# Kernel tuning notes

Measured on AMD Instinct MI355X. Metric: run time of the kernel, lower is better.

The kernel has to match this reference:

```python
import jax, jax.numpy as jnp
import numpy as np

N, DIM, HEADS, DH, WS = 32768, 1024, 8, 64, 256
INNER = HEADS * DH
MASK_VAL = -1e10  # ATTN_MASK_VALUE
EPS = 1e-5


def setup_inputs() -> dict:
    key = jax.random.key(0)
    k0, k1, k2 = jax.random.split(key, 3)
    x = jax.random.normal(k0, (N, DIM), jnp.float32)
    # rotary sin/cos with interleaved-pair layout matching rotate_every_two
    inv_freq = 1.0 / (10000.0 ** (jnp.arange(0, DH, 2, dtype=jnp.float32) / DH))
    freqs = jnp.arange(N, dtype=jnp.float32)[:, None] * inv_freq[None, :]  # [N, DH/2]
    sin = jnp.repeat(jnp.sin(freqs), 2, axis=-1)  # [N, DH]
    cos = jnp.repeat(jnp.cos(freqs), 2, axis=-1)  # [N, DH]
    gamma = jnp.ones((DIM,), jnp.float32)
    beta = jnp.zeros((DIM,), jnp.float32)
    w_qkv = jax.random.normal(k1, (DIM, 3 * INNER), jnp.float32) * 0.02
    w_out = jax.random.normal(k2, (INNER, DIM), jnp.float32) * 0.02
    b_out = jnp.zeros((DIM,), jnp.float32)
    return dict(x=x, sin=sin, cos=cos, gamma=gamma, beta=beta,
                w_qkv=w_qkv, w_out=w_out, b_out=b_out)


def _rotate_every_two(t):
    t1, t2 = t[..., 0::2], t[..., 1::2]
    return jnp.stack((-t2, t1), axis=-1).reshape(t.shape)


def _apply_rotary(t, sin, cos):
    # rot_dim == DH (full rotary), so no pass-through slice needed
    return t * cos + _rotate_every_two(t) * sin


def reference(x, sin, cos, gamma, beta, w_qkv, w_out, b_out):
    # LayerNorm (elementwise affine)
    mu = jnp.mean(x, axis=-1, keepdims=True)
    var = jnp.var(x, axis=-1, keepdims=True)
    x = (x - mu) * jax.lax.rsqrt(var + EPS) * gamma + beta
    # token shift: shift first half of channels by one token
    half = DIM // 2
    x_shift = jnp.pad(x[:, :half], ((1, 0), (0, 0)))[:-1]
    x = jnp.concatenate([x_shift, x[:, half:]], axis=-1)
    # qkv projection (no bias)
    qkv = x @ w_qkv  # [N, 3*INNER]
    q, k, v = jnp.split(qkv, 3, axis=-1)
    to_heads = lambda t: t.reshape(N, HEADS, DH).transpose(1, 0, 2)  # [H, N, DH]
    q, k, v = to_heads(q), to_heads(k), to_heads(v)
    # inline rotary on q, k AND v (as in source)
    q = _apply_rotary(q, sin, cos)
    k = _apply_rotary(k, sin, cos)
    v = _apply_rotary(v, sin, cos)
    # window split: [H, w, WS, DH]
    w = N // WS
    q, k, v = (t.reshape(HEADS, w, WS, DH) for t in (q, k, v))
    # look-back: each window attends to (previous window ++ current window)
    def lookback(t):
        t = jnp.pad(t, ((0, 0), (1, 0), (0, 0), (0, 0)))  # zero window at front
        return jnp.concatenate([t[:, :-1], t[:, 1:]], axis=2)  # [H, w, 2*WS, DH]
    k, v = lookback(k), lookback(v)
    sim = jnp.einsum('hwid,hwjd->hwij', q, k) * (DH ** -0.5)  # [H, w, WS, 2*WS]
    mask = jnp.tril(jnp.ones((WS, 2 * WS), dtype=bool), k=WS)  # j <= i + WS (causal)
    sim = jnp.where(mask, sim, MASK_VAL)
    attn = jax.nn.softmax(sim, axis=-1)
    out = jnp.einsum('hwij,hwjd->hwid', attn, v)  # [H, w, WS, DH]
    out = out.transpose(1, 2, 0, 3).reshape(N, INNER)  # '(w n) (h d)'
    return out @ w_out + b_out
```

## Files before the change

### kernel.cpp

```cpp
#include <hip/hip_runtime.h>

typedef __attribute__((ext_vector_type(4))) unsigned short us4;
typedef __attribute__((ext_vector_type(8))) unsigned short us8;
typedef __attribute__((ext_vector_type(8))) short s8;
typedef __attribute__((ext_vector_type(4))) float f32x4;
typedef __attribute__((ext_vector_type(16))) float f32x16;

#define NTOK 32768
#define DIM_ 1024
#define HEADS_ 8
#define DH_ 64
#define WS_ 256
#define NWIN_ 128
#define INNER_ 512

__device__ __forceinline__ float b2f(unsigned short u) {
  union { unsigned u; float f; } x; x.u = ((unsigned)u) << 16; return x.f;
}
__device__ __forceinline__ unsigned short f2b(float f) {
  union { float f; unsigned u; } x; x.f = f;
  unsigned r = x.u + 0x7FFFu + ((x.u >> 16) & 1u);
  return (unsigned short)(r >> 16);
}
__device__ __forceinline__ unsigned pk2(float a, float b) {
  return (unsigned)f2b(a) | ((unsigned)f2b(b) << 16);
}
__device__ __forceinline__ s8 mk_s8(unsigned w0, unsigned w1, unsigned w2, unsigned w3) {
  union { unsigned u[4]; s8 v; } x;
  x.u[0] = w0; x.u[1] = w1; x.u[2] = w2; x.u[3] = w3;
  return x.v;
}

__device__ __forceinline__ void gload_lds16(const unsigned short* g, void* l) {
  __builtin_amdgcn_global_load_lds((const __attribute__((address_space(1))) void*)g,
                                   (__attribute__((address_space(3))) void*)l, 16, 0, 0);
}

__global__ __launch_bounds__(256) void ln_shift(const float* __restrict__ x,
                                                const float* __restrict__ gamma,
                                                const float* __restrict__ beta,
                                                unsigned short* __restrict__ xs) {
  int row = blockIdx.x;
  int t = threadIdx.x;
  f32x4 v = ((const f32x4*)(x + (size_t)row * DIM_))[t];
  float sum = 0.f, ss = 0.f;
#pragma unroll
  for (int j = 0; j < 4; j++) { sum += v[j]; ss += v[j] * v[j]; }
#pragma unroll
  for (int off = 32; off >= 1; off >>= 1) {
    sum += __shfl_xor(sum, off);
    ss  += __shfl_xor(ss, off);
  }
  __shared__ float red[2][4];
  int wave = t >> 6, l = t & 63;
  if (l == 0) { red[0][wave] = sum; red[1][wave] = ss; }
  __syncthreads();
  sum = red[0][0] + red[0][1] + red[0][2] + red[0][3];
  ss  = red[1][0] + red[1][1] + red[1][2] + red[1][3];
  float mu = sum * (1.0f / DIM_);
  float var = ss * (1.0f / DIM_) - mu * mu;
  float rs = rsqrtf(var + 1e-5f);
  f32x4 g = ((const f32x4*)gamma)[t];
  f32x4 bb = ((const f32x4*)beta)[t];
  us4 o;
#pragma unroll
  for (int j = 0; j < 4; j++) o[j] = f2b((v[j] - mu) * rs * g[j] + bb[j]);
  int c0 = t * 4;
  if (c0 >= 512) {
    *(us4*)(xs + (size_t)row * DIM_ + c0) = o;
  } else {
    if (row + 1 < NTOK) *(us4*)(xs + (size_t)(row + 1) * DIM_ + c0) = o;
    if (row == 0) { us4 z = {0, 0, 0, 0}; *(us4*)(xs + c0) = z; }
  }
}

__global__ __launch_bounds__(256) void transpose_f32_bf16(const float* __restrict__ in,
                                                          unsigned short* __restrict__ out,
                                                          int R, int C) {
  __shared__ unsigned short tile[32][33];
  int bx = blockIdx.x * 32, by = blockIdx.y * 32;
  int tx = threadIdx.x, ty = threadIdx.y;
#pragma unroll
  for (int i = 0; i < 32; i += 8) tile[ty + i][tx] = f2b(in[(size_t)(by + ty + i) * C + bx + tx]);
  __syncthreads();
#pragma unroll
  for (int i = 0; i < 32; i += 8) out[(size_t)(bx + ty + i) * R + by + tx] = tile[tx][ty + i];
}

template <int MODE>
__global__ __launch_bounds__(512, 2) void gemm_p10(const unsigned short* __restrict__ A,
                                                   const unsigned short* __restrict__ Bt,
                                                   void* __restrict__ Cv,
                                                   const float* __restrict__ bias,
                                                   const float* __restrict__ sinp,
                                                   const float* __restrict__ cosp,
                                                   unsigned short* __restrict__ qh,
                                                   unsigned short* __restrict__ kh,
                                                   unsigned short* __restrict__ vt,
                                                   int M, int N, int K) {
  __shared__ __align__(16) char lds[131072];
  int t = threadIdx.x;
  int l = t & 63, lg = l >> 4, ll = l & 15;
  int wave = t >> 6;
  int wm = wave >> 2, wn = wave & 3;

  int nbx = gridDim.x;
  int nwg = nbx * gridDim.y;
  int flat = blockIdx.y * nbx + blockIdx.x;
  int swz = (flat & 7) * (nwg >> 3) + (flat >> 3);
  int m0 = (swz / nbx) * 256, n0 = (swz % nbx) * 256;

  const f32x4 fz = {0.f, 0.f, 0.f, 0.f};
  f32x4 acc[8][4];
#pragma unroll
  for (int m = 0; m < 8; m++)
#pragma unroll
    for (int n = 0; n < 4; n++) acc[m][n] = fz;

  int srow = t >> 3;
  int sunit = (t & 7) ^ (srow & 7);
  const unsigned short* gA = A + (size_t)(m0 + srow) * K + sunit * 8;
  const unsigned short* gB = Bt + (size_t)(n0 + srow) * K + sunit * 8;
  int t16 = t * 16;
  int nk = K >> 6;

#pragma unroll
  for (int j = 0; j < 4; j++) {
    gload_lds16(gA + (size_t)(j * 64) * K, lds + j * 8192 + t16);
    gload_lds16(gB + (size_t)(j * 64) * K, lds + 32768 + j * 8192 + t16);
  }

  for (int kt = 0; kt < nk - 1; ++kt) {
    const char* sa = lds + (kt & 1) * 65536;
    const char* sb = sa + 32768;
    char* dA = lds + ((kt + 1) & 1) * 65536;
    char* dB = dA + 32768;
    const unsigned short* nA = gA + (kt + 1) * 64;
    const unsigned short* nB = gB + (kt + 1) * 64;

    gload_lds16(nA, dA + t16);
    gload_lds16(nA + (size_t)64 * K, dA + 8192 + t16);
    asm volatile("s_waitcnt vmcnt(2)" ::: "memory");
    __builtin_amdgcn_sched_barrier(0);
    __builtin_amdgcn_s_barrier();
    __builtin_amdgcn_sched_barrier(0);

    s8 bf[4];
#pragma unroll
    for (int p = 0; p < 4; ++p) {
      const int qm = p & 1, kk = p >> 1;
      s8 af[4];
#pragma unroll
      for (int m = 0; m < 4; m++) {
        int r = wm * 128 + qm * 64 + m * 16 + ll;
        af[m] = *(const s8*)(sa + r * 128 + (((kk * 4 + lg) ^ (r & 7)) << 4));
      }
      if (qm == 0) {
#pragma unroll
        for (int n = 0; n < 4; n++) {
          int r = wn * 64 + n * 16 + ll;
          bf[n] = *(const s8*)(sb + r * 128 + (((kk * 4 + lg) ^ (r & 7)) << 4));
        }
      }
      if (p == 0) {
        gload_lds16(nA + (size_t)128 * K, dA + 16384 + t16);
        gload_lds16(nA + (size_t)192 * K, dA + 24576 + t16);
      } else if (p == 1) {
        gload_lds16(nB, dB + t16);
        gload_lds16(nB + (size_t)64 * K, dB + 8192 + t16);
      } else if (p == 2) {
        gload_lds16(nB + (size_t)128 * K, dB + 16384 + t16);
        gload_lds16(nB + (size_t)192 * K, dB + 24576 + t16);
      }
      __builtin_amdgcn_s_setprio(1);
#pragma unroll
      for (int m = 0; m < 4; m++)
#pragma unroll
        for (int n = 0; n < 4; n++)
          acc[qm * 4 + m][n] =
              __builtin_amdgcn_mfma_f32_16x16x32_bf16(af[m], bf[n], acc[qm * 4 + m][n], 0, 0, 0);
      __builtin_amdgcn_s_setprio(0);
    }
    __builtin_amdgcn_sched_barrier(0);
    __builtin_amdgcn_s_barrier();
  }

  {
    int kt = nk - 1;
    const char* sa = lds + (kt & 1) * 65536;
    const char* sb = sa + 32768;
    asm volatile("s_waitcnt vmcnt(0)" ::: "memory");
    __builtin_amdgcn_sched_barrier(0);
    __builtin_amdgcn_s_barrier();
    __builtin_amdgcn_sched_barrier(0);
    s8 bf[4];
#pragma unroll
    for (int p = 0; p < 4; ++p) {
      const int qm = p & 1, kk = p >> 1;
      s8 af[4];
#pragma unroll
      for (int m = 0; m < 4; m++) {
        int r = wm * 128 + qm * 64 + m * 16 + ll;
        af[m] = *(const s8*)(sa + r * 128 + (((kk * 4 + lg) ^ (r & 7)) << 4));
      }
      if (qm == 0) {
#pragma unroll
        for (int n = 0; n < 4; n++) {
          int r = wn * 64 + n * 16 + ll;
          bf[n] = *(const s8*)(sb + r * 128 + (((kk * 4 + lg) ^ (r & 7)) << 4));
        }
      }
#pragma unroll
      for (int m = 0; m < 4; m++)
#pragma unroll
        for (int n = 0; n < 4; n++)
          acc[qm * 4 + m][n] =
              __builtin_amdgcn_mfma_f32_16x16x32_bf16(af[m], bf[n], acc[qm * 4 + m][n], 0, 0, 0);
    }
  }

  if (MODE == 0) {
    int third = n0 >> 9;
    if (third == 2) {
      bool odd = (ll & 1) != 0;
#pragma unroll
      for (int m = 0; m < 8; m++) {
        int row0 = m0 + wm * 128 + m * 16 + lg * 4;
#pragma unroll
        for (int n = 0; n < 4; n++) {
          int cit = (n0 - 1024) + wn * 64 + n * 16 + ll;
          int head = cit >> 6, d = cit & 63;
          us4 st;
#pragma unroll
          for (int r = 0; r < 4; r++) {
            float v = acc[m][n][r];
            float p = __shfl_xor(v, 1);
            float sn = sinp[(size_t)(row0 + r) * 64 + d];
            float cs = cosp[(size_t)(row0 + r) * 64 + d];
            st[r] = f2b(odd ? (v * cs + p * sn) : (v * cs - p * sn));
          }
          *(us4*)(vt + ((size_t)head * 64 + d) * NTOK + row0) = st;
        }
      }
    } else {
      int b = ll & 3, q = ll >> 2;
      bool bo1 = (b & 1) != 0, bo2 = (b & 2) != 0;
#pragma unroll
      for (int m = 0; m < 8; m++) {
        int row = m0 + wm * 128 + m * 16 + lg * 4 + b;
#pragma unroll
        for (int n = 0; n < 4; n++) {
          float v0 = acc[m][n][0], v1 = acc[m][n][1], v2 = acc[m][n][2], v3 = acc[m][n][3];
          float x0 = __shfl_xor(v1, 1);
          float x1 = __shfl_xor(v0, 1);
          float x2 = __shfl_xor(v3, 1);
          float x3 = __shfl_xor(v2, 1);
          float u0 = bo1 ? x0 : v0;
          float u1 = bo1 ? v1 : x1;
          float u2 = bo1 ? x2 : v2;
          float u3 = bo1 ? v3 : x3;
          float y0 = __shfl_xor(u2, 2);
          float y1 = __shfl_xor(u3, 2);
          float y2 = __shfl_xor(u0, 2);
          float y3 = __shfl_xor(u1, 2);
          float w0 = bo2 ? y0 : u0;
          float w1 = bo2 ? y1 : u1;
          float w2 = bo2 ? u2 : y2;
          float w3 = bo2 ? u3 : y3;
          int cb = n0 + wn * 64 + n * 16 + q * 4;
          int cit = cb & 511;
          int head = cit >> 6, d0 = cit & 63;
          f32x4 s4 = *(const f32x4*)(sinp + (size_t)row * 64 + d0);
          f32x4 c4 = *(const f32x4*)(cosp + (size_t)row * 64 + d0);
          us4 st;
          st[0] = f2b(w0 * c4[0] - w1 * s4[0]);
          st[1] = f2b(w1 * c4[1] + w0 * s4[1]);
          st[2] = f2b(w2 * c4[2] - w3 * s4[2]);
          st[3] = f2b(w3 * c4[3] + w2 * s4[3]);
          if (third == 0) *(us4*)(qh + ((size_t)head * NTOK + row) * 64 + d0) = st;
          else            *(us4*)(kh + ((size_t)head * NTOK + row) * 64 + d0) = st;
        }
      }
    }
  } else {
#pragma unroll
    for (int n = 0; n < 4; n++) {
      int col = n0 + wn * 64 + n * 16 + ll;
      float bs = bias ? bias[col] : 0.0f;
#pragma unroll
      for (int m = 0; m < 8; m++) {
#pragma unroll
        for (int r = 0; r < 4; r++) {
          int row = m0 + wm * 128 + m * 16 + lg * 4 + r;
          ((float*)Cv)[(size_t)row * N + col] = acc[m][n][r] + bs;
        }
      }
    }
  }
}

__global__ __launch_bounds__(256, 4) void attn_kernel(const unsigned short* __restrict__ qh,
                                                      const unsigned short* __restrict__ kh,
                                                      const unsigned short* __restrict__ vt,
                                                      unsigned short* __restrict__ ao) {
  __shared__ char kbuf[2][8192];
  __shared__ char vbuf[8192];
  int half = blockIdx.x, w = blockIdx.y, h = blockIdx.z;
  int t = threadIdx.x;
  int wave = t >> 6, l = t & 63;
  int l31 = l & 31, hi = l >> 5;
  const unsigned short* qb = qh + (size_t)h * NTOK * 64;
  const unsigned short* kb = kh + (size_t)h * NTOK * 64;
  const unsigned short* vb = vt + (size_t)h * 64 * NTOK;

  int qw = half * 128 + wave * 32 + l31;
  int qn = w * 256 + qw;
  s8 qf[4];
#pragma unroll
  for (int dht = 0; dht < 4; dht++)
    qf[dht] = *(const s8*)(qb + (size_t)qn * 64 + dht * 16 + hi * 8);

  f32x16 o0 = {}, o1 = {};
  float dsum = (w == 0) ? 128.f : 0.f;
  int n0 = w * 256 - 256;
  int c0 = (w == 0) ? 4 : 0;

  int srow = wave * 16 + (l >> 3);
  int sunit = l & 7;

  {
    const unsigned short* g = kb + (size_t)(n0 + c0 * 64 + srow) * 64 + ((sunit ^ (srow & 7)) * 8);
    gload_lds16(g, kbuf[c0 & 1] + wave * 2048);
    gload_lds16(g + 8 * 64, kbuf[c0 & 1] + wave * 2048 + 1024);
  }
  __syncthreads();

  for (int c = c0; c < 8; ++c) {
    int cb = n0 + c * 64;
    {
      int d = srow;
      const unsigned short* g = vb + (size_t)d * NTOK + cb + ((sunit ^ (d & 7)) * 8);
      gload_lds16(g, vbuf + wave * 2048);
      gload_lds16(g + (size_t)8 * NTOK, vbuf + wave * 2048 + 1024);
    }
    if (c < 7) {
      const unsigned short* g = kb + (size_t)(cb + 64 + srow) * 64 + ((sunit ^ (srow & 7)) * 8);
      gload_lds16(g, kbuf[(c + 1) & 1] + wave * 2048);
      gload_lds16(g + 8 * 64, kbuf[(c + 1) & 1] + wave * 2048 + 1024);
    }

    f32x16 s[2] = {{}, {}};
    const char* kl = kbuf[c & 1];
#pragma unroll
    for (int kt = 0; kt < 2; kt++) {
#pragma unroll
      for (int dht = 0; dht < 4; dht++) {
        int row = kt * 32 + l31;
        int unit = (dht * 2 + hi) ^ (row & 7);
        s8 kf = *(const s8*)(kl + row * 128 + unit * 16);
        s[kt] = __builtin_amdgcn_mfma_f32_32x32x16_bf16(kf, qf[dht], s[kt], 0, 0, 0);
      }
    }

    unsigned P0[2][4], P1[2][4];
#pragma unroll
    for (int kt = 0; kt < 2; kt++) {
#pragma unroll
      for (int r = 0; r < 16; r++) {
        int j = c * 64 + kt * 32 + (r & 3) + 8 * (r >> 2) + hi * 4;
        float e = (j <= qw + 256) ? __expf(s[kt][r] * 0.125f) : 0.f;
        s[kt][r] = e;
        dsum += e;
      }
#pragma unroll
      for (int j2 = 0; j2 < 4; j2++) {
        P0[kt][j2] = pk2(s[kt][j2 * 4 + 0], s[kt][j2 * 4 + 1]);
        P1[kt][j2] = pk2(s[kt][j2 * 4 + 2], s[kt][j2 * 4 + 3]);
      }
    }

    __syncthreads();

#pragma unroll
    for (int tt = 0; tt < 4; tt++) {
      int kt = tt >> 1, ss = tt & 1;
      unsigned a = P0[kt][2 * ss], b = P1[kt][2 * ss];
      unsigned cx = P0[kt][2 * ss + 1], dx = P1[kt][2 * ss + 1];
      asm volatile("v_permlane32_swap_b32 %0, %1" : "+v"(a), "+v"(cx));
      asm volatile("v_permlane32_swap_b32 %0, %1" : "+v"(b), "+v"(dx));
      s8 pf = mk_s8(a, b, cx, dx);
      {
        int row = l31;
        int unit = (tt * 2 + hi) ^ (row & 7);
        s8 vf = *(const s8*)(vbuf + row * 128 + unit * 16);
        o0 = __builtin_amdgcn_mfma_f32_32x32x16_bf16(vf, pf, o0, 0, 0, 0);
      }
      {
        int row = 32 + l31;
        int unit = (tt * 2 + hi) ^ (row & 7);
        s8 vf = *(const s8*)(vbuf + row * 128 + unit * 16);
        o1 = __builtin_amdgcn_mfma_f32_32x32x16_bf16(vf, pf, o1, 0, 0, 0);
      }
    }
    __syncthreads();
  }

  dsum += __shfl_xor(dsum, 32);
  float inv = 1.f / dsum;

  unsigned short* orow = ao + (size_t)qn * INNER_ + h * 64;
#pragma unroll
  for (int g = 0; g < 4; g++) {
    us4 st0, st1;
#pragma unroll
    for (int rr = 0; rr < 4; rr++) {
      st0[rr] = f2b(o0[g * 4 + rr] * inv);
      st1[rr] = f2b(o1[g * 4 + rr] * inv);
    }
    *(us4*)(orow + g * 8 + hi * 4) = st0;
    *(us4*)(orow + 32 + g * 8 + hi * 4) = st1;
  }
}

extern "C" void kernel_launch(void* const* d_in, const int* in_sizes, int n_in,
                              void* d_out, int out_size, void* d_ws, size_t ws_size,
                              hipStream_t stream) {
  const float* x     = (const float*)d_in[0];
  const float* sin_  = (const float*)d_in[1];
  const float* cos_  = (const float*)d_in[2];
  const float* gamma = (const float*)d_in[3];
  const float* beta  = (const float*)d_in[4];
  const float* w_qkv = (const float*)d_in[5];
  const float* w_out = (const float*)d_in[6];
  const float* b_out = (const float*)d_in[7];

  char* ws = (char*)d_ws;
  const size_t OFF_WQT = 0;
  const size_t OFF_WOT = 3145728;
  const size_t OFF_XS  = 4194304;
  const size_t OFF_QH  = 71303168;
  const size_t OFF_KH  = 104857600;
  const size_t OFF_VT  = 138412032;
  const size_t NEEDED  = 171966464;
  if (ws_size < NEEDED) return;

  unsigned short* wqT = (unsigned short*)(ws + OFF_WQT);
  unsigned short* woT = (unsigned short*)(ws + OFF_WOT);
  unsigned short* xs  = (unsigned short*)(ws + OFF_XS);
  unsigned short* qh  = (unsigned short*)(ws + OFF_QH);
  unsigned short* kh  = (unsigned short*)(ws + OFF_KH);
  unsigned short* vt  = (unsigned short*)(ws + OFF_VT);
  unsigned short* ao  = xs;

  transpose_f32_bf16<<<dim3(1536 / 32, 1024 / 32), dim3(32, 8), 0, stream>>>(w_qkv, wqT, 1024, 1536);
  transpose_f32_bf16<<<dim3(1024 / 32, 512 / 32), dim3(32, 8), 0, stream>>>(w_out, woT, 512, 1024);
  ln_shift<<<NTOK, 256, 0, stream>>>(x, gamma, beta, xs);
  gemm_p10<0><<<dim3(1536 / 256, NTOK / 256), 512, 0, stream>>>(
      xs, wqT, nullptr, nullptr, sin_, cos_, qh, kh, vt, NTOK, 1536, 1024);
  attn_kernel<<<dim3(2, NWIN_, HEADS_), 256, 0, stream>>>(qh, kh, vt, ao);
  gemm_p10<1><<<dim3(1024 / 256, NTOK / 256), 512, 0, stream>>>(
      ao, woT, (void*)d_out, b_out, nullptr, nullptr, nullptr, nullptr, nullptr, NTOK, 1024, 512);
}
```

Measured before the change: 320.7 us.

## Triple-buffer A tiles in the GEMM to prefetch two K-steps ahead

Restructures the bf16 GEMM main loop so A tiles are triple-buffered and B tiles double-buffered in LDS (160KB total). A is now fetched two K-steps ahead and B one step ahead. All of an iteration's global-to-LDS loads are issued before a single waitcnt and barrier, instead of being interleaved with the MFMA phases. The goal is to hide more global load latency at the cost of more LDS, which is now near the per-CU limit, and of losing the fine-grained interleaving of loads with math.

```diff
diff --git a/kernel.cpp b/kernel.cpp
--- a/kernel.cpp
+++ b/kernel.cpp
@@ -87,8 +87,39 @@
   for (int i = 0; i < 32; i += 8) out[(size_t)(bx + ty + i) * R + by + tx] = tile[tx][ty + i];
 }
 
+__device__ __forceinline__ void compute_tile64(const char* sa, const char* sb,
+                                               f32x4 (&acc)[8][4],
+                                               int wm, int wn, int ll, int lg) {
+  s8 bf[4];
+#pragma unroll
+  for (int p = 0; p < 4; ++p) {
+    const int qm = p & 1, kk = p >> 1;
+    s8 af[4];
+#pragma unroll
+    for (int m = 0; m < 4; m++) {
+      int r = wm * 128 + qm * 64 + m * 16 + ll;
+      af[m] = *(const s8*)(sa + r * 128 + (((kk * 4 + lg) ^ (r & 7)) << 4));
+    }
+    if (qm == 0) {
+#pragma unroll
+      for (int n = 0; n < 4; n++) {
+        int r = wn * 64 + n * 16 + ll;
+        bf[n] = *(const s8*)(sb + r * 128 + (((kk * 4 + lg) ^ (r & 7)) << 4));
+      }
+    }
+    __builtin_amdgcn_s_setprio(1);
+#pragma unroll
+    for (int m = 0; m < 4; m++)
+#pragma unroll
+      for (int n = 0; n < 4; n++)
+        acc[qm * 4 + m][n] =
+            __builtin_amdgcn_mfma_f32_16x16x32_bf16(af[m], bf[n], acc[qm * 4 + m][n], 0, 0, 0);
+    __builtin_amdgcn_s_setprio(0);
+  }
+}
+
 template <int MODE>
-__global__ __launch_bounds__(512, 2) void gemm_p10(const unsigned short* __restrict__ A,
+__global__ __launch_bounds__(512, 2) void gemm_p11(const unsigned short* __restrict__ A,
                                                    const unsigned short* __restrict__ Bt,
                                                    void* __restrict__ Cv,
                                                    const float* __restrict__ bias,
@@ -98,7 +129,7 @@
                                                    unsigned short* __restrict__ kh,
                                                    unsigned short* __restrict__ vt,
                                                    int M, int N, int K) {
-  __shared__ __align__(16) char lds[131072];
+  __shared__ __align__(16) char lds[163840];
   int t = threadIdx.x;
   int l = t & 63, lg = l >> 4, ll = l & 15;
   int wave = t >> 6;
@@ -125,98 +156,50 @@
   int nk = K >> 6;
 
 #pragma unroll
-  for (int j = 0; j < 4; j++) {
-    gload_lds16(gA + (size_t)(j * 64) * K, lds + j * 8192 + t16);
-    gload_lds16(gB + (size_t)(j * 64) * K, lds + 32768 + j * 8192 + t16);
-  }
-
-  for (int kt = 0; kt < nk - 1; ++kt) {
-    const char* sa = lds + (kt & 1) * 65536;
-    const char* sb = sa + 32768;
-    char* dA = lds + ((kt + 1) & 1) * 65536;
-    char* dB = dA + 32768;
-    const unsigned short* nA = gA + (kt + 1) * 64;
+  for (int j = 0; j < 4; j++) gload_lds16(gA + (size_t)(j * 64) * K, lds + j * 8192 + t16);
+#pragma unroll
+  for (int j = 0; j < 4; j++) gload_lds16(gB + (size_t)(j * 64) * K, lds + 98304 + j * 8192 + t16);
+#pragma unroll
+  for (int j = 0; j < 4; j++) gload_lds16(gA + 64 + (size_t)(j * 64) * K, lds + 32768 + j * 8192 + t16);
+
+  for (int kt = 0; kt < nk - 2; ++kt) {
     const unsigned short* nB = gB + (kt + 1) * 64;
-
-    gload_lds16(nA, dA + t16);
-    gload_lds16(nA + (size_t)64 * K, dA + 8192 + t16);
-    asm volatile("s_waitcnt vmcnt(2)" ::: "memory");
+    char* dB = lds + 98304 + ((kt + 1) & 1) * 32768;
+#pragma unroll
+    for (int j = 0; j < 4; j++) gload_lds16(nB + (size_t)(j * 64) * K, dB + j * 8192 + t16);
+    const unsigned short* nA = gA + (kt + 2) * 64;
+    char* dA = lds + ((kt + 2) % 3) * 32768;
+#pragma unroll
+    for (int j = 0; j < 4; j++) gload_lds16(nA + (size_t)(j * 64) * K, dA + j * 8192 + t16);
+    asm volatile("s_waitcnt vmcnt(12)" ::: "memory");
     __builtin_amdgcn_sched_barrier(0);
     __builtin_amdgcn_s_barrier();
     __builtin_amdgcn_sched_barrier(0);
-
-    s8 bf[4];
-#pragma unroll
-    for (int p = 0; p < 4; ++p) {
-      const int qm = p & 1, kk = p >> 1;
-      s8 af[4];
-#pragma unroll
-      for (int m = 0; m < 4; m++) {
-        int r = wm * 128 + qm * 64 + m * 16 + ll;
-        af[m] = *(const s8*)(sa + r * 128 + (((kk * 4 + lg) ^ (r & 7)) << 4));
-      }
-      if (qm == 0) {
-#pragma unroll
-        for (int n = 0; n < 4; n++) {
-          int r = wn * 64 + n * 16 + ll;
-          bf[n] = *(const s8*)(sb + r * 128 + (((kk * 4 + lg) ^ (r & 7)) << 4));
-        }
-      }
-      if (p == 0) {
-        gload_lds16(nA + (size_t)128 * K, dA + 16384 + t16);
-        gload_lds16(nA + (size_t)192 * K, dA + 24576 + t16);
-      } else if (p == 1) {
-        gload_lds16(nB, dB + t16);
-        gload_lds16(nB + (size_t)64 * K, dB + 8192 + t16);
-      } else if (p == 2) {
-        gload_lds16(nB + (size_t)128 * K, dB + 16384 + t16);
-        gload_lds16(nB + (size_t)192 * K, dB + 24576 + t16);
-      }
-      __builtin_amdgcn_s_setprio(1);
-#pragma unroll
-      for (int m = 0; m < 4; m++)
-#pragma unroll
-        for (int n = 0; n < 4; n++)
-          acc[qm * 4 + m][n] =
-              __builtin_amdgcn_mfma_f32_16x16x32_bf16(af[m], bf[n], acc[qm * 4 + m][n], 0, 0, 0);
-      __builtin_amdgcn_s_setprio(0);
-    }
+    compute_tile64(lds + (kt % 3) * 32768, lds + 98304 + (kt & 1) * 32768, acc, wm, wn, ll, lg);
     __builtin_amdgcn_sched_barrier(0);
     __builtin_amdgcn_s_barrier();
   }
-
+  {
+    int kt = nk - 2;
+    const unsigned short* nB = gB + (kt + 1) * 64;
+    char* dB = lds + 98304 + ((kt + 1) & 1) * 32768;
+#pragma unroll
+    for (int j = 0; j < 4; j++) gload_lds16(nB + (size_t)(j * 64) * K, dB + j * 8192 + t16);
+    asm volatile("s_waitcnt vmcnt(8)" ::: "memory");
+    __builtin_amdgcn_sched_barrier(0);
+    __builtin_amdgcn_s_barrier();
+    __builtin_amdgcn_sched_barrier(0);
+    compute_tile64(lds + (kt % 3) * 32768, lds + 98304 + (kt & 1) * 32768, acc, wm, wn, ll, lg);
+    __builtin_amdgcn_sched_barrier(0);
+    __builtin_amdgcn_s_barrier();
+  }
   {
     int kt = nk - 1;
-    const char* sa = lds + (kt & 1) * 65536;
-    const char* sb = sa + 32768;
     asm volatile("s_waitcnt vmcnt(0)" ::: "memory");
     __builtin_amdgcn_sched_barrier(0);
     __builtin_amdgcn_s_barrier();
     __builtin_amdgcn_sched_barrier(0);
-    s8 bf[4];
-#pragma unroll
-    for (int p = 0; p < 4; ++p) {
-      const int qm = p & 1, kk = p >> 1;
-      s8 af[4];
-#pragma unroll
-      for (int m = 0; m < 4; m++) {
-        int r = wm * 128 + qm * 64 + m * 16 + ll;
-        af[m] = *(const s8*)(sa + r * 128 + (((kk * 4 + lg) ^ (r & 7)) << 4));
-      }
-      if (qm == 0) {
-#pragma unroll
-        for (int n = 0; n < 4; n++) {
-          int r = wn * 64 + n * 16 + ll;
-          bf[n] = *(const s8*)(sb + r * 128 + (((kk * 4 + lg) ^ (r & 7)) << 4));
-        }
-      }
-#pragma unroll
-      for (int m = 0; m < 4; m++)
-#pragma unroll
-        for (int n = 0; n < 4; n++)
-          acc[qm * 4 + m][n] =
-              __builtin_amdgcn_mfma_f32_16x16x32_bf16(af[m], bf[n], acc[qm * 4 + m][n], 0, 0, 0);
-    }
+    compute_tile64(lds + (kt % 3) * 32768, lds + 98304 + (kt & 1) * 32768, acc, wm, wn, ll, lg);
   }
 
   if (MODE == 0) {
@@ -455,9 +438,9 @@
   transpose_f32_bf16<<<dim3(1536 / 32, 1024 / 32), dim3(32, 8), 0, stream>>>(w_qkv, wqT, 1024, 1536);
   transpose_f32_bf16<<<dim3(1024 / 32, 512 / 32), dim3(32, 8), 0, stream>>>(w_out, woT, 512, 1024);
   ln_shift<<<NTOK, 256, 0, stream>>>(x, gamma, beta, xs);
-  gemm_p10<0><<<dim3(1536 / 256, NTOK / 256), 512, 0, stream>>>(
+  gemm_p11<0><<<dim3(1536 / 256, NTOK / 256), 512, 0, stream>>>(
       xs, wqT, nullptr, nullptr, sin_, cos_, qh, kh, vt, NTOK, 1536, 1024);
   attn_kernel<<<dim3(2, NWIN_, HEADS_), 256, 0, stream>>>(qh, kh, vt, ao);
-  gemm_p10<1><<<dim3(1024 / 256, NTOK / 256), 512, 0, stream>>>(
+  gemm_p11<1><<<dim3(1024 / 256, NTOK / 256), 512, 0, stream>>>(
       ao, woT, (void*)d_out, b_out, nullptr, nullptr, nullptr, nullptr, nullptr, NTOK, 1024, 512);
 }
```

New measurement: 329.5 us. +2.8%, slower.
